# Performance work log

Measured on AMD Instinct MI355X. Metric: run time of the kernel, lower is better.

The kernel has to match this reference:

```python
import jax, jax.numpy as jnp
import numpy as np

FRAMES = 8
NUM_HEADS = 12


def _build_indices_mask(N_origin):
    """Static (numpy) construction of gathered token indices and the
    multiplicative token mask (1.0 on allowed pairs, 0.8 elsewhere),
    matching token_mask + (1-token_mask)*0.8 in the torch code."""
    N = FRAMES * N_origin
    cls_idx = np.arange(0, N, N_origin)
    per_frame = [np.arange(i * N_origin + 1 + i, (i + 1) * N_origin, FRAMES)
                 for i in range(FRAMES)]
    idx = np.concatenate([cls_idx] + per_frame)
    M = idx.shape[0]
    mask = np.full((N, M), 0.8, dtype=np.float32)
    cls_len = cls_idx.shape[0]
    mask[:, :cls_len] = 1.0
    st = cls_len
    for i in range(FRAMES):
        ln = per_frame[i].shape[0]
        mask[i * N_origin:(i + 1) * N_origin, st:st + ln] = 1.0
        st += ln
    return jnp.asarray(idx), jnp.asarray(mask)


def setup_inputs() -> dict:
    key = jax.random.key(0)
    k1, k2, k3, k4 = jax.random.split(key, 4)
    C = 768
    x = jax.random.normal(k1, (64, 197, C), dtype=jnp.float32)
    qkv_w = jax.random.normal(k2, (3 * C, C), dtype=jnp.float32) * 0.02
    proj_w = jax.random.normal(k3, (C, C), dtype=jnp.float32) * 0.02
    proj_b = jax.random.normal(k4, (C,), dtype=jnp.float32) * 0.02
    return {"x": x, "qkv_w": qkv_w, "proj_w": proj_w, "proj_b": proj_b}


def reference(x, qkv_w, proj_w, proj_b):
    B0, N_origin, C = x.shape
    H = NUM_HEADS
    hd = C // H
    B = B0 // FRAMES
    N = FRAMES * N_origin
    scale = hd ** -0.5

    xg = x.reshape(B, N, C)                              # group 8 frames per video
    qkv = (xg @ qkv_w.T).reshape(B, N, 3, H, hd).transpose(2, 0, 3, 1, 4)
    q, k, v = qkv[0], qkv[1], qkv[2]                     # each [B, H, N, hd]

    idx, mask = _build_indices_mask(N_origin)            # idx [M], mask [N, M]
    k = k[:, :, idx, :]                                  # [B, H, M, hd]
    v = v[:, :, idx, :]

    attn = jnp.einsum('bhnd,bhmd->bhnm', q, k) * scale   # [B, H, N, M]
    attn = jax.nn.softmax(attn * mask, axis=-1)          # multiplicative mask, then softmax

    out = jnp.einsum('bhnm,bhmd->bhnd', attn, v)         # [B, H, N, hd]
    out = out.transpose(0, 2, 1, 3).reshape(B, N, C)
    out = out @ proj_w.T + proj_b
    return out.reshape(B0, N_origin, C)
```

## Files before the change

### kernel.cpp

```cpp
#include <hip/hip_runtime.h>
#include <stdint.h>

#define NORI   197
#define FRAMES 8
#define NTOK   1576
#define BATCH  8
#define NHEAD  12
#define CDIM   768
#define MG     204
#define TOKENS 12608

typedef _Float16 half8 __attribute__((ext_vector_type(8)));
typedef float floatx4 __attribute__((ext_vector_type(4)));

typedef const __attribute__((address_space(1))) void GPTR;
typedef __attribute__((address_space(3))) void LPTR;

__device__ __forceinline__ int gather_idx(int m) {
    if (m < 8) return m * NORI;
    int u = m - 8;
    int f, t;
    if (u < 100) { f = u / 25; t = u - f * 25; }
    else         { f = 4 + (u - 100) / 24; t = (u - 100) - (f - 4) * 24; }
    return f * NORI + 1 + f + 8 * t;
}
__device__ __forceinline__ int col_frame(int m) {
    int u = m - 8;
    return (u < 100) ? (u / 25) : (4 + (u - 100) / 24);
}

__global__ __launch_bounds__(256) void cast_all(
    const float* __restrict__ x, const float* __restrict__ qkvw,
    const float* __restrict__ projw, _Float16* __restrict__ out)
{
    const int n1 = TOKENS * CDIM / 8, n2 = 3 * CDIM * CDIM / 8, n3 = CDIM * CDIM / 8;
    int i = blockIdx.x * 256 + threadIdx.x;
    if (i >= n1 + n2 + n3) return;
    const float* src; int off;
    if (i < n1)           { src = x;     off = i; }
    else if (i < n1 + n2) { src = qkvw;  off = i - n1; }
    else                  { src = projw; off = i - n1 - n2; }
    float4 a = ((const float4*)src)[2 * off];
    float4 b = ((const float4*)src)[2 * off + 1];
    half8 o = { (_Float16)a.x, (_Float16)a.y, (_Float16)a.z, (_Float16)a.w,
                (_Float16)b.x, (_Float16)b.y, (_Float16)b.z, (_Float16)b.w };
    ((half8*)out)[i] = o;
}

template <int OUT_F32>
__device__ __forceinline__ void gemm_body(
    const _Float16* __restrict__ A, const _Float16* __restrict__ W,
    const float* __restrict__ bias, void* __restrict__ Y,
    int M, int Woff, int ldY, int gather, int r0, int c0,
    _Float16* As0, _Float16* Bs0, _Float16* As1, _Float16* Bs1)
{
    const int tid = threadIdx.x;
    const int w = tid >> 6, l = tid & 63;
    const int wm = (w >> 1) * 64, wn = (w & 1) * 64;

    const _Float16* sa[2];
    const _Float16* sb[2];
    int soff[2];
#pragma unroll
    for (int i = 0; i < 2; i++) {
        int rt = w * 32 + i * 16 + (l >> 2);
        int cg = (l & 3) ^ ((l >> 3) & 3);
        int ra = min(r0 + rt, M - 1);
        if (gather) { int b = ra / MG; int m = ra - b * MG; ra = b * NTOK + gather_idx(m); }
        sa[i] = A + (size_t)ra * CDIM + cg * 8;
        sb[i] = W + (size_t)(Woff + c0 + rt) * CDIM + cg * 8;
        soff[i] = (w * 32 + i * 16) * 32;
    }

#pragma unroll
    for (int i = 0; i < 2; i++) {
        __builtin_amdgcn_global_load_lds((GPTR*)sa[i], (LPTR*)(As0 + soff[i]), 16, 0, 0);
        __builtin_amdgcn_global_load_lds((GPTR*)sb[i], (LPTR*)(Bs0 + soff[i]), 16, 0, 0);
    }

    floatx4 acc[4][4] = {};
    const int fc = ((l >> 4) ^ ((l >> 1) & 3)) * 8;
    const int mrow = l & 15;

#pragma unroll
    for (int it = 0; it < 24; it++) {
        const _Float16* Ac = (it & 1) ? As1 : As0;
        const _Float16* Bc = (it & 1) ? Bs1 : Bs0;
        _Float16* An = (it & 1) ? As0 : As1;
        _Float16* Bn = (it & 1) ? Bs0 : Bs1;

        if (it < 23) {
            int kb = (it + 1) * 32;
#pragma unroll
            for (int i = 0; i < 2; i++) {
                __builtin_amdgcn_global_load_lds((GPTR*)(sa[i] + kb), (LPTR*)(An + soff[i]), 16, 0, 0);
                __builtin_amdgcn_global_load_lds((GPTR*)(sb[i] + kb), (LPTR*)(Bn + soff[i]), 16, 0, 0);
            }
            __builtin_amdgcn_s_waitcnt(0x0074);
        } else {
            __builtin_amdgcn_s_waitcnt(0x0070);
        }
        __builtin_amdgcn_s_barrier();

        half8 af[4], bf[4];
#pragma unroll
        for (int t = 0; t < 4; t++) {
            af[t] = *(const half8*)&Ac[(wm + t * 16 + mrow) * 32 + fc];
            bf[t] = *(const half8*)&Bc[(wn + t * 16 + mrow) * 32 + fc];
        }
#pragma unroll
        for (int mt = 0; mt < 4; mt++)
#pragma unroll
            for (int nt = 0; nt < 4; nt++)
                acc[mt][nt] = __builtin_amdgcn_mfma_f32_16x16x32_f16(af[mt], bf[nt], acc[mt][nt], 0, 0, 0);

        __builtin_amdgcn_s_barrier();
    }

#pragma unroll
    for (int nt = 0; nt < 4; nt++) {
        int col = c0 + wn + nt * 16 + (l & 15);
        float bv = bias ? bias[col] : 0.f;
#pragma unroll
        for (int mt = 0; mt < 4; mt++) {
#pragma unroll
            for (int r = 0; r < 4; r++) {
                int row = r0 + wm + mt * 16 + (l >> 4) * 4 + r;
                if (row < M) {
                    if (OUT_F32) ((float*)Y)[(size_t)row * ldY + col] = acc[mt][nt][r] + bv;
                    else ((_Float16*)Y)[(size_t)row * ldY + col] = (_Float16)acc[mt][nt][r];
                }
            }
        }
    }
}

__device__ __forceinline__ bool xcd_map(int bx, int nrb, int& rb, int& cb) {
    int xcd = bx & 7, j = bx >> 3;
    rb = (j % 13) * 8 + xcd;
    cb = j / 13;
    return rb < nrb;
}

__global__ __launch_bounds__(256) void gemm_qkv(
    const _Float16* __restrict__ xh, const _Float16* __restrict__ qkvwh,
    _Float16* __restrict__ Qh, _Float16* __restrict__ KVh)
{
    __shared__ __align__(16) _Float16 As0[128 * 32];
    __shared__ __align__(16) _Float16 Bs0[128 * 32];
    __shared__ __align__(16) _Float16 As1[128 * 32];
    __shared__ __align__(16) _Float16 Bs1[128 * 32];
    int bx = blockIdx.x;
    if (bx < 624) {
        int rb, cb;
        if (!xcd_map(bx, 99, rb, cb)) return;
        gemm_body<0>(xh, qkvwh, nullptr, Qh, TOKENS, 0, CDIM, 0,
                     rb * 128, cb * 128, As0, Bs0, As1, Bs1);
    } else {
        int b2 = bx - 624;
        gemm_body<0>(xh, qkvwh, nullptr, KVh, BATCH * MG, CDIM, 1536, 1,
                     (b2 / 12) * 128, (b2 % 12) * 128, As0, Bs0, As1, Bs1);
    }
}

__global__ __launch_bounds__(256) void gemm_proj(
    const _Float16* __restrict__ AOh, const _Float16* __restrict__ projwh,
    const float* __restrict__ bias, float* __restrict__ out)
{
    __shared__ __align__(16) _Float16 As0[128 * 32];
    __shared__ __align__(16) _Float16 Bs0[128 * 32];
    __shared__ __align__(16) _Float16 As1[128 * 32];
    __shared__ __align__(16) _Float16 Bs1[128 * 32];
    int rb, cb;
    if (!xcd_map(blockIdx.x, 99, rb, cb)) return;
    gemm_body<1>(AOh, projwh, bias, out, TOKENS, 0, CDIM, 0,
                 rb * 128, cb * 128, As0, Bs0, As1, Bs1);
}

__global__ __launch_bounds__(256, 2) void attn_mfma(
    const _Float16* __restrict__ Qh, const _Float16* __restrict__ KVh,
    _Float16* __restrict__ AOh)
{
    __shared__ __align__(16) _Float16 Ks[204 * 64];
    __shared__ __align__(16) _Float16 Vt[64 * 208];
    __shared__ __align__(16) _Float16 Ps[64 * 216];

    const int tid = threadIdx.x;
    const int bh = blockIdx.x;
    const int b = bh / NHEAD, h = bh - b * NHEAD;
    const int qc0 = blockIdx.y * 320;

    for (int e = tid; e < MG * 8; e += 256) {
        int row = e >> 3, c8 = e & 7;
        half8 v = *(const half8*)&KVh[(size_t)(b * MG + row) * 1536 + h * 64 + c8 * 8];
        *(half8*)&Ks[row * 64 + ((c8 ^ (row & 7)) * 8)] = v;
    }
    {
        const int d0 = (tid >> 5) * 8, lmp = tid & 31;
#pragma unroll
        for (int mo = 0; mo < 7; mo++) {
            int mp = mo * 32 + lmp;
            if (mp >= 208) continue;
            half8 v = {};
            if (mp < MG) v = *(const half8*)&KVh[(size_t)(b * MG + mp) * 1536 + 768 + h * 64 + d0];
#pragma unroll
            for (int j = 0; j < 8; j++) Vt[(d0 + j) * 208 + mp] = v[j];
        }
    }
    __syncthreads();

    const int w = tid >> 6, l = tid & 63;
    const int lm = l & 15, lq = l >> 4;

    int cf[13];
#pragma unroll
    for (int t = 0; t < 13; t++) {
        int col = t * 16 + lm;
        cf[t] = (col < 8) ? -1 : (col >= MG ? -2 : col_frame(col));
    }

    _Float16* Pw = &Ps[(w * 16) * 216];

    for (int t5 = 0; t5 < 5; t5++) {
        const int rb = qc0 + t5 * 64 + w * 16;
        if (rb >= NTOK) break;

        floatx4 acc[13] = {};
        const int qrowA = min(rb + lm, NTOK - 1);
        const _Float16* qbase = Qh + (size_t)(b * NTOK + qrowA) * CDIM + h * 64;
#pragma unroll
        for (int ks = 0; ks < 64; ks += 32) {
            half8 aq = *(const half8*)(qbase + ks + lq * 8);
#pragma unroll
            for (int t = 0; t < 13; t++) {
                half8 bk = *(const half8*)&Ks[(t * 16 + lm) * 64 + (((ks >> 3) + lq) ^ (lm & 7)) * 8];
                acc[t] = __builtin_amdgcn_mfma_f32_16x16x32_f16(aq, bk, acc[t], 0, 0, 0);
            }
        }

#pragma unroll
        for (int r = 0; r < 4; r++) {
            int qrow = min(rb + lq * 4 + r, NTOK - 1);
            int rf = qrow / NORI;
            float sv[13];
            float mx = -1e30f;
#pragma unroll
            for (int t = 0; t < 13; t++) {
                float s = acc[t][r] * 0.125f;
                s *= (cf[t] == -1 || cf[t] == rf) ? 1.f : 0.8f;
                if (cf[t] == -2) s = -1e30f;
                sv[t] = s;
                mx = fmaxf(mx, s);
            }
#pragma unroll
            for (int off = 1; off < 16; off <<= 1) mx = fmaxf(mx, __shfl_xor(mx, off, 64));
            float sum = 0.f;
#pragma unroll
            for (int t = 0; t < 13; t++) { sv[t] = __expf(sv[t] - mx); sum += sv[t]; }
#pragma unroll
            for (int off = 1; off < 16; off <<= 1) sum += __shfl_xor(sum, off, 64);
            float inv = 1.f / sum;
#pragma unroll
            for (int t = 0; t < 13; t++) acc[t][r] = sv[t] * inv;
        }

#pragma unroll
        for (int t = 0; t < 13; t++)
#pragma unroll
            for (int r = 0; r < 4; r++)
                Pw[(lq * 4 + r) * 216 + t * 16 + lm] = (_Float16)acc[t][r];

        floatx4 oacc[4] = {};
        const _Float16* prow = &Pw[lm * 216];
#pragma unroll
        for (int ks = 0; ks < 192; ks += 32) {
            half8 ap = *(const half8*)(prow + ks + lq * 8);
#pragma unroll
            for (int t = 0; t < 4; t++) {
                half8 bv = *(const half8*)&Vt[(t * 16 + lm) * 208 + ks + lq * 8];
                oacc[t] = __builtin_amdgcn_mfma_f32_16x16x32_f16(ap, bv, oacc[t], 0, 0, 0);
            }
        }
        {
            typedef _Float16 half4v __attribute__((ext_vector_type(4)));
            half4v ap4 = *(const half4v*)(prow + 192 + lq * 4);
#pragma unroll
            for (int t = 0; t < 4; t++) {
                half4v bv4 = *(const half4v*)&Vt[(t * 16 + lm) * 208 + 192 + lq * 4];
                oacc[t] = __builtin_amdgcn_mfma_f32_16x16x16f16(ap4, bv4, oacc[t], 0, 0, 0);
            }
        }

#pragma unroll
        for (int t = 0; t < 4; t++)
#pragma unroll
            for (int r = 0; r < 4; r++) {
                int qrow = rb + lq * 4 + r;
                if (qrow < NTOK)
                    AOh[(size_t)(b * NTOK + qrow) * CDIM + h * 64 + t * 16 + lm] = (_Float16)oacc[t][r];
            }
    }
}

extern "C" void kernel_launch(void* const* d_in, const int* in_sizes, int n_in,
                              void* d_out, int out_size, void* d_ws, size_t ws_size,
                              hipStream_t stream) {
    const float* x      = (const float*)d_in[0];
    const float* qkv_w  = (const float*)d_in[1];
    const float* proj_w = (const float*)d_in[2];
    const float* proj_b = (const float*)d_in[3];
    float* out = (float*)d_out;

    _Float16* xh     = (_Float16*)d_ws;
    _Float16* qkvwh  = xh + (size_t)TOKENS * CDIM;
    _Float16* projwh = qkvwh + (size_t)3 * CDIM * CDIM;
    _Float16* Qh     = projwh + (size_t)CDIM * CDIM;
    _Float16* KVh    = Qh + (size_t)TOKENS * CDIM;
    _Float16* AOh    = KVh + (size_t)(BATCH * MG) * 1536;

    dim3 blk(256);
    const int ncast = (TOKENS * CDIM + 3 * CDIM * CDIM + CDIM * CDIM) / 8;
    cast_all<<<dim3((ncast + 255) / 256), blk, 0, stream>>>(x, qkv_w, proj_w, xh);

    gemm_qkv<<<dim3(624 + 156), blk, 0, stream>>>(xh, qkvwh, Qh, KVh);

    attn_mfma<<<dim3(BATCH * NHEAD, 5), blk, 0, stream>>>(Qh, KVh, AOh);

    gemm_proj<<<dim3(624), blk, 0, stream>>>(AOh, projwh, proj_b, out);
}
```

Before: 187.2 us.

## Fuse fp32-to-fp16 cast of x into QKV GEMM A-tile loads

```diff
diff --git a/kernel.cpp b/kernel.cpp
--- a/kernel.cpp
+++ b/kernel.cpp
@@ -29,17 +29,16 @@
     return (u < 100) ? (u / 25) : (4 + (u - 100) / 24);
 }
 
-__global__ __launch_bounds__(256) void cast_all(
-    const float* __restrict__ x, const float* __restrict__ qkvw,
-    const float* __restrict__ projw, _Float16* __restrict__ out)
-{
-    const int n1 = TOKENS * CDIM / 8, n2 = 3 * CDIM * CDIM / 8, n3 = CDIM * CDIM / 8;
+__global__ __launch_bounds__(256) void cast_w(
+    const float* __restrict__ qkvw, const float* __restrict__ projw,
+    _Float16* __restrict__ out)
+{
+    const int n2 = 3 * CDIM * CDIM / 8, n3 = CDIM * CDIM / 8;
     int i = blockIdx.x * 256 + threadIdx.x;
-    if (i >= n1 + n2 + n3) return;
+    if (i >= n2 + n3) return;
     const float* src; int off;
-    if (i < n1)           { src = x;     off = i; }
-    else if (i < n1 + n2) { src = qkvw;  off = i - n1; }
-    else                  { src = projw; off = i - n1 - n2; }
+    if (i < n2) { src = qkvw;  off = i; }
+    else        { src = projw; off = i - n2; }
     float4 a = ((const float4*)src)[2 * off];
     float4 b = ((const float4*)src)[2 * off + 1];
     half8 o = { (_Float16)a.x, (_Float16)a.y, (_Float16)a.z, (_Float16)a.w,
@@ -47,9 +46,21 @@
     ((half8*)out)[i] = o;
 }
 
-template <int OUT_F32>
+#define LOADA(R, K)                                                            \
+    do { _Pragma("unroll") for (int i = 0; i < 2; i++) {                       \
+        R[i][0] = ((const float4*)(saf[i] + (K) * 32))[0];                     \
+        R[i][1] = ((const float4*)(saf[i] + (K) * 32))[1]; } } while (0)
+#define CVTWR(R, DST)                                                          \
+    do { _Pragma("unroll") for (int i = 0; i < 2; i++) {                       \
+        half8 h = { (_Float16)R[i][0].x, (_Float16)R[i][0].y,                  \
+                    (_Float16)R[i][0].z, (_Float16)R[i][0].w,                  \
+                    (_Float16)R[i][1].x, (_Float16)R[i][1].y,                  \
+                    (_Float16)R[i][1].z, (_Float16)R[i][1].w };                \
+        *(half8*)&DST[soff[i] + l * 8] = h; } } while (0)
+
+template <int OUT_F32, int A_F32>
 __device__ __forceinline__ void gemm_body(
-    const _Float16* __restrict__ A, const _Float16* __restrict__ W,
+    const void* __restrict__ Ain, const _Float16* __restrict__ W,
     const float* __restrict__ bias, void* __restrict__ Y,
     int M, int Woff, int ldY, int gather, int r0, int c0,
     _Float16* As0, _Float16* Bs0, _Float16* As1, _Float16* Bs1)
@@ -59,6 +70,7 @@
     const int wm = (w >> 1) * 64, wn = (w & 1) * 64;
 
     const _Float16* sa[2];
+    const float* saf[2];
     const _Float16* sb[2];
     int soff[2];
 #pragma unroll
@@ -67,15 +79,28 @@
         int cg = (l & 3) ^ ((l >> 3) & 3);
         int ra = min(r0 + rt, M - 1);
         if (gather) { int b = ra / MG; int m = ra - b * MG; ra = b * NTOK + gather_idx(m); }
-        sa[i] = A + (size_t)ra * CDIM + cg * 8;
+        if (A_F32) saf[i] = (const float*)Ain + (size_t)ra * CDIM + cg * 8;
+        else       sa[i]  = (const _Float16*)Ain + (size_t)ra * CDIM + cg * 8;
         sb[i] = W + (size_t)(Woff + c0 + rt) * CDIM + cg * 8;
         soff[i] = (w * 32 + i * 16) * 32;
     }
 
-#pragma unroll
-    for (int i = 0; i < 2; i++) {
-        __builtin_amdgcn_global_load_lds((GPTR*)sa[i], (LPTR*)(As0 + soff[i]), 16, 0, 0);
-        __builtin_amdgcn_global_load_lds((GPTR*)sb[i], (LPTR*)(Bs0 + soff[i]), 16, 0, 0);
+    float4 arA[2][2], arB[2][2];
+
+    if (A_F32) {
+        LOADA(arA, 0);
+        __builtin_amdgcn_s_waitcnt(0x0070);
+        CVTWR(arA, As0);
+        LOADA(arB, 1);
+#pragma unroll
+        for (int i = 0; i < 2; i++)
+            __builtin_amdgcn_global_load_lds((GPTR*)sb[i], (LPTR*)(Bs0 + soff[i]), 16, 0, 0);
+    } else {
+#pragma unroll
+        for (int i = 0; i < 2; i++) {
+            __builtin_amdgcn_global_load_lds((GPTR*)sa[i], (LPTR*)(As0 + soff[i]), 16, 0, 0);
+            __builtin_amdgcn_global_load_lds((GPTR*)sb[i], (LPTR*)(Bs0 + soff[i]), 16, 0, 0);
+        }
     }
 
     floatx4 acc[4][4] = {};
@@ -89,16 +114,34 @@
         _Float16* An = (it & 1) ? As0 : As1;
         _Float16* Bn = (it & 1) ? Bs0 : Bs1;
 
-        if (it < 23) {
-            int kb = (it + 1) * 32;
-#pragma unroll
-            for (int i = 0; i < 2; i++) {
-                __builtin_amdgcn_global_load_lds((GPTR*)(sa[i] + kb), (LPTR*)(An + soff[i]), 16, 0, 0);
-                __builtin_amdgcn_global_load_lds((GPTR*)(sb[i] + kb), (LPTR*)(Bn + soff[i]), 16, 0, 0);
-            }
-            __builtin_amdgcn_s_waitcnt(0x0074);
+        if (A_F32) {
+            if (it < 23) {
+                __builtin_amdgcn_s_waitcnt(0x0072);
+                if (it & 1) { CVTWR(arA, An); } else { CVTWR(arB, An); }
+                if (it < 22) {
+                    if (it & 1) { LOADA(arB, it + 2); } else { LOADA(arA, it + 2); }
+                }
+#pragma unroll
+                for (int i = 0; i < 2; i++)
+                    __builtin_amdgcn_global_load_lds((GPTR*)(sb[i] + (it + 1) * 32),
+                                                     (LPTR*)(Bn + soff[i]), 16, 0, 0);
+                if (it < 22) __builtin_amdgcn_s_waitcnt(0x0076);
+                else         __builtin_amdgcn_s_waitcnt(0x0072);
+            } else {
+                __builtin_amdgcn_s_waitcnt(0x0070);
+            }
         } else {
-            __builtin_amdgcn_s_waitcnt(0x0070);
+            if (it < 23) {
+                int kb = (it + 1) * 32;
+#pragma unroll
+                for (int i = 0; i < 2; i++) {
+                    __builtin_amdgcn_global_load_lds((GPTR*)(sa[i] + kb), (LPTR*)(An + soff[i]), 16, 0, 0);
+                    __builtin_amdgcn_global_load_lds((GPTR*)(sb[i] + kb), (LPTR*)(Bn + soff[i]), 16, 0, 0);
+                }
+                __builtin_amdgcn_s_waitcnt(0x0074);
+            } else {
+                __builtin_amdgcn_s_waitcnt(0x0070);
+            }
         }
         __builtin_amdgcn_s_barrier();
 
@@ -142,8 +185,8 @@
     return rb < nrb;
 }
 
-__global__ __launch_bounds__(256) void gemm_qkv(
-    const _Float16* __restrict__ xh, const _Float16* __restrict__ qkvwh,
+__global__ __launch_bounds__(256, 3) void gemm_qkv(
+    const float* __restrict__ x, const _Float16* __restrict__ qkvwh,
     _Float16* __restrict__ Qh, _Float16* __restrict__ KVh)
 {
     __shared__ __align__(16) _Float16 As0[128 * 32];
@@ -154,12 +197,12 @@
     if (bx < 624) {
         int rb, cb;
         if (!xcd_map(bx, 99, rb, cb)) return;
-        gemm_body<0>(xh, qkvwh, nullptr, Qh, TOKENS, 0, CDIM, 0,
-                     rb * 128, cb * 128, As0, Bs0, As1, Bs1);
+        gemm_body<0, 1>(x, qkvwh, nullptr, Qh, TOKENS, 0, CDIM, 0,
+                        rb * 128, cb * 128, As0, Bs0, As1, Bs1);
     } else {
         int b2 = bx - 624;
-        gemm_body<0>(xh, qkvwh, nullptr, KVh, BATCH * MG, CDIM, 1536, 1,
-                     (b2 / 12) * 128, (b2 % 12) * 128, As0, Bs0, As1, Bs1);
+        gemm_body<0, 1>(x, qkvwh, nullptr, KVh, BATCH * MG, CDIM, 1536, 1,
+                        (b2 / 12) * 128, (b2 % 12) * 128, As0, Bs0, As1, Bs1);
     }
 }
 
@@ -173,8 +216,8 @@
     __shared__ __align__(16) _Float16 Bs1[128 * 32];
     int rb, cb;
     if (!xcd_map(blockIdx.x, 99, rb, cb)) return;
-    gemm_body<1>(AOh, projwh, bias, out, TOKENS, 0, CDIM, 0,
-                 rb * 128, cb * 128, As0, Bs0, As1, Bs1);
+    gemm_body<1, 0>(AOh, projwh, bias, out, TOKENS, 0, CDIM, 0,
+                    rb * 128, cb * 128, As0, Bs0, As1, Bs1);
 }
 
 __global__ __launch_bounds__(256, 2) void attn_mfma(
@@ -228,6 +271,7 @@
         floatx4 acc[13] = {};
         const int qrowA = min(rb + lm, NTOK - 1);
         const _Float16* qbase = Qh + (size_t)(b * NTOK + qrowA) * CDIM + h * 64;
+        __builtin_amdgcn_s_setprio(1);
 #pragma unroll
         for (int ks = 0; ks < 64; ks += 32) {
             half8 aq = *(const half8*)(qbase + ks + lq * 8);
@@ -237,6 +281,7 @@
                 acc[t] = __builtin_amdgcn_mfma_f32_16x16x32_f16(aq, bk, acc[t], 0, 0, 0);
             }
         }
+        __builtin_amdgcn_s_setprio(0);
 
 #pragma unroll
         for (int r = 0; r < 4; r++) {
@@ -272,6 +317,7 @@
 
         floatx4 oacc[4] = {};
         const _Float16* prow = &Pw[lm * 216];
+        __builtin_amdgcn_s_setprio(1);
 #pragma unroll
         for (int ks = 0; ks < 192; ks += 32) {
             half8 ap = *(const half8*)(prow + ks + lq * 8);
@@ -290,6 +336,7 @@
                 oacc[t] = __builtin_amdgcn_mfma_f32_16x16x16f16(ap4, bv4, oacc[t], 0, 0, 0);
             }
         }
+        __builtin_amdgcn_s_setprio(0);
 
 #pragma unroll
         for (int t = 0; t < 4; t++)
@@ -311,18 +358,17 @@
     const float* proj_b = (const float*)d_in[3];
     float* out = (float*)d_out;
 
-    _Float16* xh     = (_Float16*)d_ws;
-    _Float16* qkvwh  = xh + (size_t)TOKENS * CDIM;
+    _Float16* qkvwh  = (_Float16*)d_ws;
     _Float16* projwh = qkvwh + (size_t)3 * CDIM * CDIM;
     _Float16* Qh     = projwh + (size_t)CDIM * CDIM;
     _Float16* KVh    = Qh + (size_t)TOKENS * CDIM;
     _Float16* AOh    = KVh + (size_t)(BATCH * MG) * 1536;
 
     dim3 blk(256);
-    const int ncast = (TOKENS * CDIM + 3 * CDIM * CDIM + CDIM * CDIM) / 8;
-    cast_all<<<dim3((ncast + 255) / 256), blk, 0, stream>>>(x, qkv_w, proj_w, xh);
-
-    gemm_qkv<<<dim3(624 + 156), blk, 0, stream>>>(xh, qkvwh, Qh, KVh);
+    const int ncast = (3 * CDIM * CDIM + CDIM * CDIM) / 8;
+    cast_w<<<dim3((ncast + 255) / 256), blk, 0, stream>>>(qkv_w, proj_w, qkvwh);
+
+    gemm_qkv<<<dim3(624 + 156), blk, 0, stream>>>(x, qkvwh, Qh, KVh);
 
     attn_mfma<<<dim3(BATCH * NHEAD, 5), blk, 0, stream>>>(Qh, KVh, AOh);
 
```

New measurement: 191.3 us. +2.2%, slower.

## Shrink GEMM M-tile to 64 rows, remap workgroups per XCD, prioritize attention MFMA

Applied to the files above, without the earlier changes.

```diff
diff --git a/kernel.cpp b/kernel.cpp
--- a/kernel.cpp
+++ b/kernel.cpp
@@ -48,7 +48,7 @@
 }
 
 template <int OUT_F32>
-__device__ __forceinline__ void gemm_body(
+__device__ __forceinline__ void gemm_body64(
     const _Float16* __restrict__ A, const _Float16* __restrict__ W,
     const float* __restrict__ bias, void* __restrict__ Y,
     int M, int Woff, int ldY, int gather, int r0, int c0,
@@ -56,31 +56,36 @@
 {
     const int tid = threadIdx.x;
     const int w = tid >> 6, l = tid & 63;
-    const int wm = (w >> 1) * 64, wn = (w & 1) * 64;
-
-    const _Float16* sa[2];
+    const int wm = (w >> 1) * 32, wn = (w & 1) * 64;
+    const int cg = (l & 3) ^ ((l >> 3) & 3);
+
+    const _Float16* saA;
+    {
+        int rt = w * 16 + (l >> 2);
+        int ra = min(r0 + rt, M - 1);
+        if (gather) { int b = ra / MG; int m = ra - b * MG; ra = b * NTOK + gather_idx(m); }
+        saA = A + (size_t)ra * CDIM + cg * 8;
+    }
+    const int soffA = (w * 16) * 32;
+
     const _Float16* sb[2];
-    int soff[2];
+    int soffB[2];
 #pragma unroll
     for (int i = 0; i < 2; i++) {
         int rt = w * 32 + i * 16 + (l >> 2);
-        int cg = (l & 3) ^ ((l >> 3) & 3);
-        int ra = min(r0 + rt, M - 1);
-        if (gather) { int b = ra / MG; int m = ra - b * MG; ra = b * NTOK + gather_idx(m); }
-        sa[i] = A + (size_t)ra * CDIM + cg * 8;
         sb[i] = W + (size_t)(Woff + c0 + rt) * CDIM + cg * 8;
-        soff[i] = (w * 32 + i * 16) * 32;
-    }
-
-#pragma unroll
-    for (int i = 0; i < 2; i++) {
-        __builtin_amdgcn_global_load_lds((GPTR*)sa[i], (LPTR*)(As0 + soff[i]), 16, 0, 0);
-        __builtin_amdgcn_global_load_lds((GPTR*)sb[i], (LPTR*)(Bs0 + soff[i]), 16, 0, 0);
-    }
-
-    floatx4 acc[4][4] = {};
+        soffB[i] = (w * 32 + i * 16) * 32;
+    }
+
+    __builtin_amdgcn_global_load_lds((GPTR*)saA, (LPTR*)(As0 + soffA), 16, 0, 0);
+#pragma unroll
+    for (int i = 0; i < 2; i++)
+        __builtin_amdgcn_global_load_lds((GPTR*)sb[i], (LPTR*)(Bs0 + soffB[i]), 16, 0, 0);
+
+    floatx4 acc[2][4] = {};
     const int fc = ((l >> 4) ^ ((l >> 1) & 3)) * 8;
     const int mrow = l & 15;
+    const int lm = l & 15, lq = l >> 4;
 
 #pragma unroll
     for (int it = 0; it < 24; it++) {
@@ -91,41 +96,43 @@
 
         if (it < 23) {
             int kb = (it + 1) * 32;
-#pragma unroll
-            for (int i = 0; i < 2; i++) {
-                __builtin_amdgcn_global_load_lds((GPTR*)(sa[i] + kb), (LPTR*)(An + soff[i]), 16, 0, 0);
-                __builtin_amdgcn_global_load_lds((GPTR*)(sb[i] + kb), (LPTR*)(Bn + soff[i]), 16, 0, 0);
-            }
-            __builtin_amdgcn_s_waitcnt(0x0074);
+            __builtin_amdgcn_global_load_lds((GPTR*)(saA + kb), (LPTR*)(An + soffA), 16, 0, 0);
+#pragma unroll
+            for (int i = 0; i < 2; i++)
+                __builtin_amdgcn_global_load_lds((GPTR*)(sb[i] + kb), (LPTR*)(Bn + soffB[i]), 16, 0, 0);
+            __builtin_amdgcn_s_waitcnt(0x0073);
         } else {
             __builtin_amdgcn_s_waitcnt(0x0070);
         }
         __builtin_amdgcn_s_barrier();
-
-        half8 af[4], bf[4];
-#pragma unroll
-        for (int t = 0; t < 4; t++) {
+        __builtin_amdgcn_sched_barrier(0);
+
+        half8 af[2], bf[4];
+#pragma unroll
+        for (int t = 0; t < 2; t++)
             af[t] = *(const half8*)&Ac[(wm + t * 16 + mrow) * 32 + fc];
+#pragma unroll
+        for (int t = 0; t < 4; t++)
             bf[t] = *(const half8*)&Bc[(wn + t * 16 + mrow) * 32 + fc];
-        }
-#pragma unroll
-        for (int mt = 0; mt < 4; mt++)
+#pragma unroll
+        for (int mt = 0; mt < 2; mt++)
 #pragma unroll
             for (int nt = 0; nt < 4; nt++)
                 acc[mt][nt] = __builtin_amdgcn_mfma_f32_16x16x32_f16(af[mt], bf[nt], acc[mt][nt], 0, 0, 0);
 
+        __builtin_amdgcn_sched_barrier(0);
         __builtin_amdgcn_s_barrier();
     }
 
 #pragma unroll
     for (int nt = 0; nt < 4; nt++) {
-        int col = c0 + wn + nt * 16 + (l & 15);
+        int col = c0 + wn + nt * 16 + lm;
         float bv = bias ? bias[col] : 0.f;
 #pragma unroll
-        for (int mt = 0; mt < 4; mt++) {
+        for (int mt = 0; mt < 2; mt++) {
 #pragma unroll
             for (int r = 0; r < 4; r++) {
-                int row = r0 + wm + mt * 16 + (l >> 4) * 4 + r;
+                int row = r0 + wm + mt * 16 + lq * 4 + r;
                 if (row < M) {
                     if (OUT_F32) ((float*)Y)[(size_t)row * ldY + col] = acc[mt][nt][r] + bv;
                     else ((_Float16*)Y)[(size_t)row * ldY + col] = (_Float16)acc[mt][nt][r];
@@ -135,46 +142,48 @@
     }
 }
 
-__device__ __forceinline__ bool xcd_map(int bx, int nrb, int& rb, int& cb) {
-    int xcd = bx & 7, j = bx >> 3;
-    rb = (j % 13) * 8 + xcd;
-    cb = j / 13;
-    return rb < nrb;
-}
-
-__global__ __launch_bounds__(256) void gemm_qkv(
+__device__ __forceinline__ int xcd_chunk(int bid, int nwg) {
+    int xcd = bid & 7, j = bid >> 3;
+    int q = nwg >> 3, r = nwg & 7;
+    int base = (xcd < r) ? xcd * (q + 1) : r * (q + 1) + (xcd - r) * q;
+    return base + j;
+}
+
+__global__ __launch_bounds__(256, 5) void gemm_qkv(
     const _Float16* __restrict__ xh, const _Float16* __restrict__ qkvwh,
     _Float16* __restrict__ Qh, _Float16* __restrict__ KVh)
 {
-    __shared__ __align__(16) _Float16 As0[128 * 32];
+    __shared__ __align__(16) _Float16 As0[64 * 32];
     __shared__ __align__(16) _Float16 Bs0[128 * 32];
-    __shared__ __align__(16) _Float16 As1[128 * 32];
+    __shared__ __align__(16) _Float16 As1[64 * 32];
     __shared__ __align__(16) _Float16 Bs1[128 * 32];
     int bx = blockIdx.x;
-    if (bx < 624) {
-        int rb, cb;
-        if (!xcd_map(bx, 99, rb, cb)) return;
-        gemm_body<0>(xh, qkvwh, nullptr, Qh, TOKENS, 0, CDIM, 0,
-                     rb * 128, cb * 128, As0, Bs0, As1, Bs1);
+    if (bx < 1182) {
+        int wg = xcd_chunk(bx, 1182);
+        int rb = wg / 6, cb = wg - rb * 6;
+        gemm_body64<0>(xh, qkvwh, nullptr, Qh, TOKENS, 0, CDIM, 0,
+                       rb * 64, cb * 128, As0, Bs0, As1, Bs1);
     } else {
-        int b2 = bx - 624;
-        gemm_body<0>(xh, qkvwh, nullptr, KVh, BATCH * MG, CDIM, 1536, 1,
-                     (b2 / 12) * 128, (b2 % 12) * 128, As0, Bs0, As1, Bs1);
-    }
-}
-
-__global__ __launch_bounds__(256) void gemm_proj(
+        int b2 = bx - 1182;
+        int wg = xcd_chunk(b2, 312);
+        int rb = wg / 12, cb = wg - rb * 12;
+        gemm_body64<0>(xh, qkvwh, nullptr, KVh, BATCH * MG, CDIM, 1536, 1,
+                       rb * 64, cb * 128, As0, Bs0, As1, Bs1);
+    }
+}
+
+__global__ __launch_bounds__(256, 5) void gemm_proj(
     const _Float16* __restrict__ AOh, const _Float16* __restrict__ projwh,
     const float* __restrict__ bias, float* __restrict__ out)
 {
-    __shared__ __align__(16) _Float16 As0[128 * 32];
+    __shared__ __align__(16) _Float16 As0[64 * 32];
     __shared__ __align__(16) _Float16 Bs0[128 * 32];
-    __shared__ __align__(16) _Float16 As1[128 * 32];
+    __shared__ __align__(16) _Float16 As1[64 * 32];
     __shared__ __align__(16) _Float16 Bs1[128 * 32];
-    int rb, cb;
-    if (!xcd_map(blockIdx.x, 99, rb, cb)) return;
-    gemm_body<1>(AOh, projwh, bias, out, TOKENS, 0, CDIM, 0,
-                 rb * 128, cb * 128, As0, Bs0, As1, Bs1);
+    int wg = xcd_chunk(blockIdx.x, 1182);
+    int rb = wg / 6, cb = wg - rb * 6;
+    gemm_body64<1>(AOh, projwh, bias, out, TOKENS, 0, CDIM, 0,
+                   rb * 64, cb * 128, As0, Bs0, As1, Bs1);
 }
 
 __global__ __launch_bounds__(256, 2) void attn_mfma(
@@ -228,6 +237,7 @@
         floatx4 acc[13] = {};
         const int qrowA = min(rb + lm, NTOK - 1);
         const _Float16* qbase = Qh + (size_t)(b * NTOK + qrowA) * CDIM + h * 64;
+        __builtin_amdgcn_s_setprio(1);
 #pragma unroll
         for (int ks = 0; ks < 64; ks += 32) {
             half8 aq = *(const half8*)(qbase + ks + lq * 8);
@@ -237,6 +247,7 @@
                 acc[t] = __builtin_amdgcn_mfma_f32_16x16x32_f16(aq, bk, acc[t], 0, 0, 0);
             }
         }
+        __builtin_amdgcn_s_setprio(0);
 
 #pragma unroll
         for (int r = 0; r < 4; r++) {
@@ -272,6 +283,7 @@
 
         floatx4 oacc[4] = {};
         const _Float16* prow = &Pw[lm * 216];
+        __builtin_amdgcn_s_setprio(1);
 #pragma unroll
         for (int ks = 0; ks < 192; ks += 32) {
             half8 ap = *(const half8*)(prow + ks + lq * 8);
@@ -290,6 +302,7 @@
                 oacc[t] = __builtin_amdgcn_mfma_f32_16x16x16f16(ap4, bv4, oacc[t], 0, 0, 0);
             }
         }
+        __builtin_amdgcn_s_setprio(0);
 
 #pragma unroll
         for (int t = 0; t < 4; t++)
@@ -322,9 +335,9 @@
     const int ncast = (TOKENS * CDIM + 3 * CDIM * CDIM + CDIM * CDIM) / 8;
     cast_all<<<dim3((ncast + 255) / 256), blk, 0, stream>>>(x, qkv_w, proj_w, xh);
 
-    gemm_qkv<<<dim3(624 + 156), blk, 0, stream>>>(xh, qkvwh, Qh, KVh);
+    gemm_qkv<<<dim3(1182 + 312), blk, 0, stream>>>(xh, qkvwh, Qh, KVh);
 
     attn_mfma<<<dim3(BATCH * NHEAD, 5), blk, 0, stream>>>(Qh, KVh, AOh);
 
-    gemm_proj<<<dim3(624), blk, 0, stream>>>(AOh, projwh, proj_b, out);
-}
+    gemm_proj<<<dim3(1182), blk, 0, stream>>>(AOh, projwh, proj_b, out);
+}
```

After: 187.7 us. No clear change (+0.3%).

## Remap workgroups to XCD-contiguous chunks and add scheduling barriers and priorities

Applied to the files above, without the earlier changes.

```diff
diff --git a/kernel.cpp b/kernel.cpp
--- a/kernel.cpp
+++ b/kernel.cpp
@@ -29,12 +29,23 @@
     return (u < 100) ? (u / 25) : (4 + (u - 100) / 24);
 }
 
+__device__ __forceinline__ int xcd_chunk(int bid, int nwg) {
+    int xcd = bid & 7, j = bid >> 3;
+    int q = nwg >> 3, r = nwg & 7;
+    int base = (xcd < r) ? xcd * (q + 1) : r * (q + 1) + (xcd - r) * q;
+    return base + j;
+}
+
 __global__ __launch_bounds__(256) void cast_all(
     const float* __restrict__ x, const float* __restrict__ qkvw,
     const float* __restrict__ projw, _Float16* __restrict__ out)
 {
     const int n1 = TOKENS * CDIM / 8, n2 = 3 * CDIM * CDIM / 8, n3 = CDIM * CDIM / 8;
-    int i = blockIdx.x * 256 + threadIdx.x;
+    const int nxb = n1 / 256;
+    int bx = blockIdx.x;
+    int i;
+    if (bx < nxb) i = xcd_chunk(bx, nxb) * 256 + threadIdx.x;
+    else          i = bx * 256 + threadIdx.x;
     if (i >= n1 + n2 + n3) return;
     const float* src; int off;
     if (i < n1)           { src = x;     off = i; }
@@ -101,6 +112,7 @@
             __builtin_amdgcn_s_waitcnt(0x0070);
         }
         __builtin_amdgcn_s_barrier();
+        __builtin_amdgcn_sched_barrier(0);
 
         half8 af[4], bf[4];
 #pragma unroll
@@ -114,6 +126,7 @@
             for (int nt = 0; nt < 4; nt++)
                 acc[mt][nt] = __builtin_amdgcn_mfma_f32_16x16x32_f16(af[mt], bf[nt], acc[mt][nt], 0, 0, 0);
 
+        __builtin_amdgcn_sched_barrier(0);
         __builtin_amdgcn_s_barrier();
     }
 
@@ -135,13 +148,6 @@
     }
 }
 
-__device__ __forceinline__ bool xcd_map(int bx, int nrb, int& rb, int& cb) {
-    int xcd = bx & 7, j = bx >> 3;
-    rb = (j % 13) * 8 + xcd;
-    cb = j / 13;
-    return rb < nrb;
-}
-
 __global__ __launch_bounds__(256) void gemm_qkv(
     const _Float16* __restrict__ xh, const _Float16* __restrict__ qkvwh,
     _Float16* __restrict__ Qh, _Float16* __restrict__ KVh)
@@ -151,15 +157,18 @@
     __shared__ __align__(16) _Float16 As1[128 * 32];
     __shared__ __align__(16) _Float16 Bs1[128 * 32];
     int bx = blockIdx.x;
-    if (bx < 624) {
-        int rb, cb;
-        if (!xcd_map(bx, 99, rb, cb)) return;
+    if (bx < 600) {
+        if (bx >= 594) return;
+        int wg = xcd_chunk(bx, 594);
+        int rb = wg / 6, cb = wg - rb * 6;
         gemm_body<0>(xh, qkvwh, nullptr, Qh, TOKENS, 0, CDIM, 0,
                      rb * 128, cb * 128, As0, Bs0, As1, Bs1);
     } else {
-        int b2 = bx - 624;
+        int b2 = bx - 600;
+        int wg = xcd_chunk(b2, 156);
+        int rb = wg / 12, cb = wg - rb * 12;
         gemm_body<0>(xh, qkvwh, nullptr, KVh, BATCH * MG, CDIM, 1536, 1,
-                     (b2 / 12) * 128, (b2 % 12) * 128, As0, Bs0, As1, Bs1);
+                     rb * 128, cb * 128, As0, Bs0, As1, Bs1);
     }
 }
 
@@ -171,8 +180,8 @@
     __shared__ __align__(16) _Float16 Bs0[128 * 32];
     __shared__ __align__(16) _Float16 As1[128 * 32];
     __shared__ __align__(16) _Float16 Bs1[128 * 32];
-    int rb, cb;
-    if (!xcd_map(blockIdx.x, 99, rb, cb)) return;
+    int wg = xcd_chunk(blockIdx.x, 594);
+    int rb = wg / 6, cb = wg - rb * 6;
     gemm_body<1>(AOh, projwh, bias, out, TOKENS, 0, CDIM, 0,
                  rb * 128, cb * 128, As0, Bs0, As1, Bs1);
 }
@@ -186,9 +195,11 @@
     __shared__ __align__(16) _Float16 Ps[64 * 216];
 
     const int tid = threadIdx.x;
-    const int bh = blockIdx.x;
-    const int b = bh / NHEAD, h = bh - b * NHEAD;
-    const int qc0 = blockIdx.y * 320;
+    const int id = blockIdx.x;
+    const int b = id & 7;
+    const int j = id >> 3;
+    const int h = j % NHEAD;
+    const int qc0 = (j / NHEAD) * 320;
 
     for (int e = tid; e < MG * 8; e += 256) {
         int row = e >> 3, c8 = e & 7;
@@ -204,7 +215,7 @@
             half8 v = {};
             if (mp < MG) v = *(const half8*)&KVh[(size_t)(b * MG + mp) * 1536 + 768 + h * 64 + d0];
 #pragma unroll
-            for (int j = 0; j < 8; j++) Vt[(d0 + j) * 208 + mp] = v[j];
+            for (int jj = 0; jj < 8; jj++) Vt[(d0 + jj) * 208 + mp] = v[jj];
         }
     }
     __syncthreads();
@@ -228,6 +239,7 @@
         floatx4 acc[13] = {};
         const int qrowA = min(rb + lm, NTOK - 1);
         const _Float16* qbase = Qh + (size_t)(b * NTOK + qrowA) * CDIM + h * 64;
+        __builtin_amdgcn_s_setprio(1);
 #pragma unroll
         for (int ks = 0; ks < 64; ks += 32) {
             half8 aq = *(const half8*)(qbase + ks + lq * 8);
@@ -237,6 +249,7 @@
                 acc[t] = __builtin_amdgcn_mfma_f32_16x16x32_f16(aq, bk, acc[t], 0, 0, 0);
             }
         }
+        __builtin_amdgcn_s_setprio(0);
 
 #pragma unroll
         for (int r = 0; r < 4; r++) {
@@ -272,6 +285,7 @@
 
         floatx4 oacc[4] = {};
         const _Float16* prow = &Pw[lm * 216];
+        __builtin_amdgcn_s_setprio(1);
 #pragma unroll
         for (int ks = 0; ks < 192; ks += 32) {
             half8 ap = *(const half8*)(prow + ks + lq * 8);
@@ -290,6 +304,7 @@
                 oacc[t] = __builtin_amdgcn_mfma_f32_16x16x16f16(ap4, bv4, oacc[t], 0, 0, 0);
             }
         }
+        __builtin_amdgcn_s_setprio(0);
 
 #pragma unroll
         for (int t = 0; t < 4; t++)
@@ -322,9 +337,9 @@
     const int ncast = (TOKENS * CDIM + 3 * CDIM * CDIM + CDIM * CDIM) / 8;
     cast_all<<<dim3((ncast + 255) / 256), blk, 0, stream>>>(x, qkv_w, proj_w, xh);
 
-    gemm_qkv<<<dim3(624 + 156), blk, 0, stream>>>(xh, qkvwh, Qh, KVh);
-
-    attn_mfma<<<dim3(BATCH * NHEAD, 5), blk, 0, stream>>>(Qh, KVh, AOh);
-
-    gemm_proj<<<dim3(624), blk, 0, stream>>>(AOh, projwh, proj_b, out);
-}
+    gemm_qkv<<<dim3(600 + 156), blk, 0, stream>>>(xh, qkvwh, Qh, KVh);
+
+    attn_mfma<<<dim3(480), blk, 0, stream>>>(Qh, KVh, AOh);
+
+    gemm_proj<<<dim3(594), blk, 0, stream>>>(AOh, projwh, proj_b, out);
+}
```

Measured after the change: 181.8 us (median of 2 runs). -2.9%, faster.
